# Optimization experiments

Hardware: AMD Instinct MI355X
Metric: run time of the kernel (lower is better)

## Reference

```python
import jax, jax.numpy as jnp
import numpy as np

EMBED_DIM = 768
NUM_HEADS = 12
HEAD_SIZE = EMBED_DIM // NUM_HEADS


def setup_inputs() -> dict:
    key = jax.random.key(0)
    ks = jax.random.split(key, 9)
    B, S, D = 4, 2048, EMBED_DIM
    scale = 1.0 / np.sqrt(D)
    x = jax.random.normal(ks[0], (B, S, D), dtype=jnp.float32)
    # Linear params (torch nn.Linear: y = x @ W.T + b); store W as [in, out] for einsum
    Wq = jax.random.normal(ks[1], (D, D), dtype=jnp.float32) * scale
    bq = jnp.zeros((D,), dtype=jnp.float32)
    Wk = jax.random.normal(ks[2], (D, D), dtype=jnp.float32) * scale
    bk = jnp.zeros((D,), dtype=jnp.float32)
    Wv = jax.random.normal(ks[3], (D, D), dtype=jnp.float32) * scale
    bv = jnp.zeros((D,), dtype=jnp.float32)
    Wo = jax.random.normal(ks[4], (D, D), dtype=jnp.float32) * scale
    bo = jnp.zeros((D,), dtype=jnp.float32)
    return {"x": x, "Wq": Wq, "bq": bq, "Wk": Wk, "bk": bk,
            "Wv": Wv, "bv": bv, "Wo": Wo, "bo": bo}


def reference(x, Wq, bq, Wk, bk, Wv, bv, Wo, bo):
    B, S, D = x.shape
    H, hs = NUM_HEADS, HEAD_SIZE
    scale = hs ** (-0.5)
    # Projections
    Q = (x @ Wq + bq).reshape(B, S, H, hs)
    K = (x @ Wk + bk).reshape(B, S, H, hs)
    V = (x @ Wv + bv).reshape(B, S, H, hs)
    # Batched attention over all heads (equivalent to the per-head loop:
    # torch view splits last dim into H contiguous chunks; concat of per-head
    # outputs along -1 restores the same layout)
    scores = jnp.einsum('bqhd,bkhd->bhqk', Q, K) * scale  # [B,H,S,S]
    attn = jax.nn.softmax(scores, axis=-1)
    out = jnp.einsum('bhqk,bkhd->bqhd', attn, V).reshape(B, S, D)
    # Output projection; dropout is identity in eval mode
    return out @ Wo + bo
```

## Files before the change

### kernel.cpp

```cpp
#include <hip/hip_runtime.h>

typedef unsigned short ushort_t;
typedef __bf16 bf16x8 __attribute__((ext_vector_type(8)));
typedef float floatx4 __attribute__((ext_vector_type(4)));

__device__ inline ushort_t f2bf(float f) {
    __bf16 h = (__bf16)f;
    return __builtin_bit_cast(ushort_t, h);
}

__device__ inline void gload16(const void* g, void* l) {
    __builtin_amdgcn_global_load_lds((const __attribute__((address_space(1))) void*)g,
                                     (__attribute__((address_space(3))) void*)l, 16, 0, 0);
}

__global__ __launch_bounds__(256) void prep_kernel(
    const float* __restrict__ x, ushort_t* __restrict__ xbf,
    const float* __restrict__ W0, const float* __restrict__ W1,
    const float* __restrict__ W2, const float* __restrict__ W3,
    ushort_t* __restrict__ T0, ushort_t* __restrict__ T1,
    ushort_t* __restrict__ T2, ushort_t* __restrict__ T3) {
    int bx = blockIdx.x;
    int tid = threadIdx.x;
    if (bx < 2304) {
        __shared__ float t[32][33];
        int w = bx / 576, rem = bx % 576;
        const float* W; ushort_t* T;
        switch (w) {
            case 0: W = W0; T = T0; break;
            case 1: W = W1; T = T1; break;
            case 2: W = W2; T = T2; break;
            default: W = W3; T = T3; break;
        }
        int n0 = (rem / 24) * 32, k0 = (rem % 24) * 32;
        int tx = tid & 31, ty = tid >> 5;
        for (int i = 0; i < 4; ++i)
            t[ty + i * 8][tx] = W[(k0 + ty + i * 8) * 768 + n0 + tx];
        __syncthreads();
        for (int i = 0; i < 4; ++i)
            T[(n0 + ty + i * 8) * 768 + k0 + tx] = f2bf(t[tx][ty + i * 8]);
    } else {
        int i = ((bx - 2304) * 256 + tid) * 4;
        float4 v = *(const float4*)(x + i);
        ushort4 u;
        u.x = f2bf(v.x); u.y = f2bf(v.y); u.z = f2bf(v.z); u.w = f2bf(v.w);
        *(ushort4*)(xbf + i) = u;
    }
}

__global__ __launch_bounds__(256) void gemm_qkv(
    const ushort_t* __restrict__ A,
    const ushort_t* __restrict__ Tq, const ushort_t* __restrict__ Tk, const ushort_t* __restrict__ Tv,
    const float* __restrict__ bq, const float* __restrict__ bk, const float* __restrict__ bv,
    ushort_t* __restrict__ Qb, ushort_t* __restrict__ Kb, ushort_t* __restrict__ Vtb) {
    __shared__ ushort_t sh[128 * 64 + 64 * 64];
    ushort_t* As = sh;
    ushort_t* Bs = sh + 128 * 64;
    int tid = threadIdx.x;
    int m0 = blockIdx.x * 128;
    int by = blockIdx.y;
    int which = by / 12;
    int n0 = (by % 12) * 64;
    const ushort_t* Bt = which == 0 ? Tq : (which == 1 ? Tk : Tv);
    const float* bias = which == 0 ? bq : (which == 1 ? bk : bv);

    int wave = tid >> 6;
    int lane = tid & 63;
    int ln = tid & 15;
    int quad = (tid >> 4) & 3;
    int wm = wave * 32;
    int lr = lane >> 3;
    int lc = (lane & 7) * 8;

    floatx4 acc[2][4];
    floatx4 z = {0.f, 0.f, 0.f, 0.f};
    for (int i = 0; i < 2; ++i)
        for (int j = 0; j < 4; ++j) acc[i][j] = z;

    for (int kt = 0; kt < 12; ++kt) {
        int k0 = kt * 64;
        __syncthreads();
        for (int i = 0; i < 4; ++i) {
            int c = wave * 4 + i;
            gload16(&A[(m0 + c * 8 + lr) * 768 + k0 + lc], &As[c * 512]);
        }
        for (int i = 0; i < 2; ++i) {
            int c = wave * 2 + i;
            gload16(&Bt[(n0 + c * 8 + lr) * 768 + k0 + lc], &Bs[c * 512]);
        }
        __syncthreads();
        for (int ks = 0; ks < 2; ++ks) {
            bf16x8 a[2], b[4];
            for (int i = 0; i < 2; ++i)
                a[i] = *(const bf16x8*)&As[(wm + i * 16 + ln) * 64 + ks * 32 + quad * 8];
            for (int j = 0; j < 4; ++j)
                b[j] = *(const bf16x8*)&Bs[(j * 16 + ln) * 64 + ks * 32 + quad * 8];
            for (int i = 0; i < 2; ++i)
                for (int j = 0; j < 4; ++j)
                    acc[i][j] = __builtin_amdgcn_mfma_f32_16x16x32_bf16(a[i], b[j], acc[i][j], 0, 0, 0);
        }
    }

    const float QSCALE = 0.125f * 1.44269504088896f;
    if (which != 2) {
        for (int i = 0; i < 2; ++i) {
            for (int j = 0; j < 4; ++j) {
                int gn = n0 + j * 16 + ln;
                float bia = bias[gn];
                int h = gn >> 6, dd = gn & 63;
                for (int r = 0; r < 4; ++r) {
                    int gm = m0 + wm + i * 16 + quad * 4 + r;
                    int bb = gm >> 11, ss = gm & 2047;
                    float v = acc[i][j][r] + bia;
                    if (which == 0) {
                        Qb[((bb * 12 + h) * 2048 + ss) * 64 + dd] = f2bf(v * QSCALE);
                    } else {
                        Kb[((bb * 12 + h) * 2048 + ss) * 64 + dd] = f2bf(v);
                    }
                }
            }
        }
    } else {
        __syncthreads();
        ushort_t* tr = sh;
        for (int j = 0; j < 4; ++j) {
            int nl = j * 16 + ln;
            float bia = bias[n0 + nl];
            for (int i = 0; i < 2; ++i) {
                ushort4 u;
                u.x = f2bf(acc[i][j][0] + bia);
                u.y = f2bf(acc[i][j][1] + bia);
                u.z = f2bf(acc[i][j][2] + bia);
                u.w = f2bf(acc[i][j][3] + bia);
                *(ushort4*)&tr[nl * 136 + wm + i * 16 + quad * 4] = u;
            }
        }
        __syncthreads();
        int bb = m0 >> 11, ss0 = m0 & 2047;
        int head = by % 12;
        for (int p = 0; p < 4; ++p) {
            int n = p * 16 + (tid >> 4);
            int mc = (tid & 15) * 8;
            uint4 v = *(const uint4*)&tr[n * 136 + mc];
            *(uint4*)&Vtb[(size_t)((bb * 12 + head) * 64 + n) * 2048 + ss0 + mc] = v;
        }
    }
}

__global__ __launch_bounds__(256) void attn_kernel(
    const ushort_t* __restrict__ Qb, const ushort_t* __restrict__ Kb,
    const ushort_t* __restrict__ Vtb, ushort_t* __restrict__ Ob) {
    __shared__ ushort_t Ks[2][64 * 72];
    __shared__ ushort_t Vs[2][64 * 72];
    int tid = threadIdx.x;
    int bid = blockIdx.x;
    int swz = (bid & 7) * 96 + (bid >> 3);
    int bh = swz >> 4;
    int qt = swz & 15;
    int wave = tid >> 6;
    int ln = tid & 15;
    int quad = (tid >> 4) & 3;
    int q0 = qt * 128 + wave * 32;

    const ushort_t* Qp = Qb + (size_t)bh * 2048 * 64;
    const ushort_t* Kp = Kb + (size_t)bh * 2048 * 64;
    const ushort_t* Vp = Vtb + (size_t)bh * 64 * 2048;

    bf16x8 bqf[2][2];
    for (int g = 0; g < 2; ++g)
        for (int ks = 0; ks < 2; ++ks)
            bqf[g][ks] = *(const bf16x8*)&Qp[(q0 + g * 16 + ln) * 64 + ks * 32 + quad * 8];

    int srow = tid >> 3;
    int c8 = tid & 7;
    int scol = c8 * 8;
    int u = c8 & 3;
    int vcol = (c8 >> 2) * 32 + (u & 1) * 16 + (u >> 1) * 4;

    uint4 kreg[2], vreg[2];

    for (int p = 0; p < 2; ++p) {
        kreg[p] = *(const uint4*)&Kp[(p * 32 + srow) * 64 + scol];
        vreg[p] = *(const uint4*)&Vp[(p * 32 + srow) * 2048 + scol];
    }
    for (int p = 0; p < 2; ++p) {
        *(uint4*)&Ks[0][(p * 32 + srow) * 72 + scol] = kreg[p];
        ushort_t* vb = &Vs[0][(p * 32 + srow) * 72 + vcol];
        *(uint2*)vb = make_uint2(vreg[p].x, vreg[p].y);
        *(uint2*)(vb + 8) = make_uint2(vreg[p].z, vreg[p].w);
    }
    __syncthreads();

    floatx4 o_acc[2][4];
    float lsum[2] = {0.f, 0.f};
    floatx4 z = {0.f, 0.f, 0.f, 0.f};
    for (int g = 0; g < 2; ++g)
        for (int m4 = 0; m4 < 4; ++m4) o_acc[g][m4] = z;

    for (int kt = 0; kt < 32; ++kt) {
        int cur = kt & 1;
        if (kt < 31) {
            for (int p = 0; p < 2; ++p) {
                kreg[p] = *(const uint4*)&Kp[((kt + 1) * 64 + p * 32 + srow) * 64 + scol];
                vreg[p] = *(const uint4*)&Vp[(p * 32 + srow) * 2048 + (kt + 1) * 64 + scol];
            }
        }

        const ushort_t* KsH = Ks[cur];
        const ushort_t* VsH = Vs[cur];

        bf16x8 ak[4][2];
        for (int m4 = 0; m4 < 4; ++m4)
            for (int ks = 0; ks < 2; ++ks)
                ak[m4][ks] = *(const bf16x8*)&KsH[(m4 * 16 + ln) * 72 + ks * 32 + quad * 8];

        floatx4 st[2][4];
        for (int g = 0; g < 2; ++g)
            for (int m4 = 0; m4 < 4; ++m4) {
                floatx4 s = z;
                s = __builtin_amdgcn_mfma_f32_16x16x32_bf16(ak[m4][0], bqf[g][0], s, 0, 0, 0);
                s = __builtin_amdgcn_mfma_f32_16x16x32_bf16(ak[m4][1], bqf[g][1], s, 0, 0, 0);
                st[g][m4] = s;
            }

        float pv[2][4][4];
        for (int g = 0; g < 2; ++g)
            for (int m4 = 0; m4 < 4; ++m4)
                for (int r = 0; r < 4; ++r) {
                    float e = __builtin_amdgcn_exp2f(st[g][m4][r]);
                    pv[g][m4][r] = e;
                    lsum[g] += e;
                }

        bf16x8 av[4][2];
        for (int m4 = 0; m4 < 4; ++m4)
            for (int c = 0; c < 2; ++c)
                av[m4][c] = *(const bf16x8*)&VsH[(m4 * 16 + ln) * 72 + c * 32 + quad * 8];

        for (int g = 0; g < 2; ++g) {
            bf16x8 bp[2];
            for (int c = 0; c < 2; ++c) {
                bf16x8 b;
                b[0] = (__bf16)pv[g][2 * c][0];
                b[1] = (__bf16)pv[g][2 * c][1];
                b[2] = (__bf16)pv[g][2 * c][2];
                b[3] = (__bf16)pv[g][2 * c][3];
                b[4] = (__bf16)pv[g][2 * c + 1][0];
                b[5] = (__bf16)pv[g][2 * c + 1][1];
                b[6] = (__bf16)pv[g][2 * c + 1][2];
                b[7] = (__bf16)pv[g][2 * c + 1][3];
                bp[c] = b;
            }
            for (int m4 = 0; m4 < 4; ++m4)
                for (int c = 0; c < 2; ++c)
                    o_acc[g][m4] = __builtin_amdgcn_mfma_f32_16x16x32_bf16(av[m4][c], bp[c], o_acc[g][m4], 0, 0, 0);
        }

        if (kt < 31) {
            int nxt = cur ^ 1;
            for (int p = 0; p < 2; ++p) {
                *(uint4*)&Ks[nxt][(p * 32 + srow) * 72 + scol] = kreg[p];
                ushort_t* vb = &Vs[nxt][(p * 32 + srow) * 72 + vcol];
                *(uint2*)vb = make_uint2(vreg[p].x, vreg[p].y);
                *(uint2*)(vb + 8) = make_uint2(vreg[p].z, vreg[p].w);
            }
        }
        __syncthreads();
    }

    for (int g = 0; g < 2; ++g) {
        lsum[g] += __shfl_xor(lsum[g], 16);
        lsum[g] += __shfl_xor(lsum[g], 32);
    }

    int b = bh / 12, h = bh % 12;
    for (int g = 0; g < 2; ++g) {
        float inv = 1.f / lsum[g];
        int token = b * 2048 + q0 + g * 16 + ln;
        for (int m4 = 0; m4 < 4; ++m4)
            for (int r = 0; r < 4; ++r)
                Ob[token * 768 + h * 64 + m4 * 16 + quad * 4 + r] = f2bf(o_acc[g][m4][r] * inv);
    }
}

__global__ __launch_bounds__(256) void gemm_out(
    const ushort_t* __restrict__ A, const ushort_t* __restrict__ Bt,
    const float* __restrict__ bias, float* __restrict__ out) {
    __shared__ ushort_t As[128 * 64];
    __shared__ ushort_t Bs[64 * 64];
    int tid = threadIdx.x;
    int m0 = blockIdx.x * 128;
    int n0 = blockIdx.y * 64;

    int wave = tid >> 6;
    int lane = tid & 63;
    int ln = tid & 15;
    int quad = (tid >> 4) & 3;
    int wm = wave * 32;
    int lr = lane >> 3;
    int lc = (lane & 7) * 8;

    floatx4 acc[2][4];
    floatx4 z = {0.f, 0.f, 0.f, 0.f};
    for (int i = 0; i < 2; ++i)
        for (int j = 0; j < 4; ++j) acc[i][j] = z;

    for (int kt = 0; kt < 12; ++kt) {
        int k0 = kt * 64;
        __syncthreads();
        for (int i = 0; i < 4; ++i) {
            int c = wave * 4 + i;
            gload16(&A[(m0 + c * 8 + lr) * 768 + k0 + lc], &As[c * 512]);
        }
        for (int i = 0; i < 2; ++i) {
            int c = wave * 2 + i;
            gload16(&Bt[(n0 + c * 8 + lr) * 768 + k0 + lc], &Bs[c * 512]);
        }
        __syncthreads();
        for (int ks = 0; ks < 2; ++ks) {
            bf16x8 a[2], b[4];
            for (int i = 0; i < 2; ++i)
                a[i] = *(const bf16x8*)&As[(wm + i * 16 + ln) * 64 + ks * 32 + quad * 8];
            for (int j = 0; j < 4; ++j)
                b[j] = *(const bf16x8*)&Bs[(j * 16 + ln) * 64 + ks * 32 + quad * 8];
            for (int i = 0; i < 2; ++i)
                for (int j = 0; j < 4; ++j)
                    acc[i][j] = __builtin_amdgcn_mfma_f32_16x16x32_bf16(a[i], b[j], acc[i][j], 0, 0, 0);
        }
    }

    for (int i = 0; i < 2; ++i) {
        for (int j = 0; j < 4; ++j) {
            int gn = n0 + j * 16 + ln;
            float bia = bias[gn];
            for (int r = 0; r < 4; ++r) {
                int gm = m0 + wm + i * 16 + quad * 4 + r;
                out[gm * 768 + gn] = acc[i][j][r] + bia;
            }
        }
    }
}

extern "C" void kernel_launch(void* const* d_in, const int* in_sizes, int n_in,
                              void* d_out, int out_size, void* d_ws, size_t ws_size,
                              hipStream_t stream) {
    const float* x  = (const float*)d_in[0];
    const float* Wq = (const float*)d_in[1];
    const float* bq = (const float*)d_in[2];
    const float* Wk = (const float*)d_in[3];
    const float* bk = (const float*)d_in[4];
    const float* Wv = (const float*)d_in[5];
    const float* bv = (const float*)d_in[6];
    const float* Wo = (const float*)d_in[7];
    const float* bo = (const float*)d_in[8];

    const int NTOK = 4 * 2048;
    const int NELT = NTOK * 768;
    const int WELT = 768 * 768;

    ushort_t* xbf = (ushort_t*)d_ws;
    ushort_t* Tq  = xbf + NELT;
    ushort_t* Tk  = Tq + WELT;
    ushort_t* Tv  = Tk + WELT;
    ushort_t* To  = Tv + WELT;
    ushort_t* Qb  = To + WELT;
    ushort_t* Kb  = Qb + NELT;
    ushort_t* Vtb = Kb + NELT;
    ushort_t* Ob  = Vtb + NELT;

    prep_kernel<<<8448, 256, 0, stream>>>(x, xbf, Wq, Wk, Wv, Wo, Tq, Tk, Tv, To);
    gemm_qkv<<<dim3(64, 36), 256, 0, stream>>>(xbf, Tq, Tk, Tv, bq, bk, bv, Qb, Kb, Vtb);
    attn_kernel<<<768, 256, 0, stream>>>(Qb, Kb, Vtb, Ob);
    gemm_out<<<dim3(64, 12), 256, 0, stream>>>(Ob, To, bo, (float*)d_out);
}
```

Baseline: 222.2 us.

## Split attention key tile across wave pairs and reduce partial outputs in LDS

Reorganizes the attention kernel's four waves into 2 query groups × 2 key halves. Each wave now handles 64 queries against 32 of the 64 keys per tile, which halves the per-wave LDS fragment reads of K and V while keeping the MFMA count the same. After the loop, the second key-half wave writes its partial output and row sums into reused shared memory, and the first wave combines them and normalizes. The cost is doubled Q and accumulator registers per wave and an extra LDS reduction with a barrier. The float scratch buffer reaches past the Ks array into Vs, so it relies on the two arrays being laid out contiguously.

```diff
diff --git a/kernel.cpp b/kernel.cpp
--- a/kernel.cpp
+++ b/kernel.cpp
@@ -158,16 +158,18 @@
     int bh = swz >> 4;
     int qt = swz & 15;
     int wave = tid >> 6;
+    int qh = wave >> 1;
+    int kh = wave & 1;
     int ln = tid & 15;
     int quad = (tid >> 4) & 3;
-    int q0 = qt * 128 + wave * 32;
+    int q0 = qt * 128 + qh * 64;
 
     const ushort_t* Qp = Qb + (size_t)bh * 2048 * 64;
     const ushort_t* Kp = Kb + (size_t)bh * 2048 * 64;
     const ushort_t* Vp = Vtb + (size_t)bh * 64 * 2048;
 
-    bf16x8 bqf[2][2];
-    for (int g = 0; g < 2; ++g)
+    bf16x8 bqf[4][2];
+    for (int g = 0; g < 4; ++g)
         for (int ks = 0; ks < 2; ++ks)
             bqf[g][ks] = *(const bf16x8*)&Qp[(q0 + g * 16 + ln) * 64 + ks * 32 + quad * 8];
 
@@ -191,10 +193,10 @@
     }
     __syncthreads();
 
-    floatx4 o_acc[2][4];
-    float lsum[2] = {0.f, 0.f};
+    floatx4 o_acc[4][4];
+    float lsum[4] = {0.f, 0.f, 0.f, 0.f};
     floatx4 z = {0.f, 0.f, 0.f, 0.f};
-    for (int g = 0; g < 2; ++g)
+    for (int g = 0; g < 4; ++g)
         for (int m4 = 0; m4 < 4; ++m4) o_acc[g][m4] = z;
 
     for (int kt = 0; kt < 32; ++kt) {
@@ -209,51 +211,45 @@
         const ushort_t* KsH = Ks[cur];
         const ushort_t* VsH = Vs[cur];
 
-        bf16x8 ak[4][2];
-        for (int m4 = 0; m4 < 4; ++m4)
+        bf16x8 ak[2][2];
+        for (int m = 0; m < 2; ++m)
             for (int ks = 0; ks < 2; ++ks)
-                ak[m4][ks] = *(const bf16x8*)&KsH[(m4 * 16 + ln) * 72 + ks * 32 + quad * 8];
-
-        floatx4 st[2][4];
-        for (int g = 0; g < 2; ++g)
-            for (int m4 = 0; m4 < 4; ++m4) {
+                ak[m][ks] = *(const bf16x8*)&KsH[((kh * 2 + m) * 16 + ln) * 72 + ks * 32 + quad * 8];
+
+        floatx4 st[4][2];
+        for (int g = 0; g < 4; ++g)
+            for (int m = 0; m < 2; ++m) {
                 floatx4 s = z;
-                s = __builtin_amdgcn_mfma_f32_16x16x32_bf16(ak[m4][0], bqf[g][0], s, 0, 0, 0);
-                s = __builtin_amdgcn_mfma_f32_16x16x32_bf16(ak[m4][1], bqf[g][1], s, 0, 0, 0);
-                st[g][m4] = s;
-            }
-
-        float pv[2][4][4];
-        for (int g = 0; g < 2; ++g)
-            for (int m4 = 0; m4 < 4; ++m4)
+                s = __builtin_amdgcn_mfma_f32_16x16x32_bf16(ak[m][0], bqf[g][0], s, 0, 0, 0);
+                s = __builtin_amdgcn_mfma_f32_16x16x32_bf16(ak[m][1], bqf[g][1], s, 0, 0, 0);
+                st[g][m] = s;
+            }
+
+        float pv[4][2][4];
+        for (int g = 0; g < 4; ++g)
+            for (int m = 0; m < 2; ++m)
                 for (int r = 0; r < 4; ++r) {
-                    float e = __builtin_amdgcn_exp2f(st[g][m4][r]);
-                    pv[g][m4][r] = e;
+                    float e = __builtin_amdgcn_exp2f(st[g][m][r]);
+                    pv[g][m][r] = e;
                     lsum[g] += e;
                 }
 
-        bf16x8 av[4][2];
+        bf16x8 av[4];
         for (int m4 = 0; m4 < 4; ++m4)
-            for (int c = 0; c < 2; ++c)
-                av[m4][c] = *(const bf16x8*)&VsH[(m4 * 16 + ln) * 72 + c * 32 + quad * 8];
-
-        for (int g = 0; g < 2; ++g) {
-            bf16x8 bp[2];
-            for (int c = 0; c < 2; ++c) {
-                bf16x8 b;
-                b[0] = (__bf16)pv[g][2 * c][0];
-                b[1] = (__bf16)pv[g][2 * c][1];
-                b[2] = (__bf16)pv[g][2 * c][2];
-                b[3] = (__bf16)pv[g][2 * c][3];
-                b[4] = (__bf16)pv[g][2 * c + 1][0];
-                b[5] = (__bf16)pv[g][2 * c + 1][1];
-                b[6] = (__bf16)pv[g][2 * c + 1][2];
-                b[7] = (__bf16)pv[g][2 * c + 1][3];
-                bp[c] = b;
-            }
+            av[m4] = *(const bf16x8*)&VsH[(m4 * 16 + ln) * 72 + kh * 32 + quad * 8];
+
+        for (int g = 0; g < 4; ++g) {
+            bf16x8 b;
+            b[0] = (__bf16)pv[g][0][0];
+            b[1] = (__bf16)pv[g][0][1];
+            b[2] = (__bf16)pv[g][0][2];
+            b[3] = (__bf16)pv[g][0][3];
+            b[4] = (__bf16)pv[g][1][0];
+            b[5] = (__bf16)pv[g][1][1];
+            b[6] = (__bf16)pv[g][1][2];
+            b[7] = (__bf16)pv[g][1][3];
             for (int m4 = 0; m4 < 4; ++m4)
-                for (int c = 0; c < 2; ++c)
-                    o_acc[g][m4] = __builtin_amdgcn_mfma_f32_16x16x32_bf16(av[m4][c], bp[c], o_acc[g][m4], 0, 0, 0);
+                o_acc[g][m4] = __builtin_amdgcn_mfma_f32_16x16x32_bf16(av[m4], b, o_acc[g][m4], 0, 0, 0);
         }
 
         if (kt < 31) {
@@ -268,18 +264,36 @@
         __syncthreads();
     }
 
-    for (int g = 0; g < 2; ++g) {
+    for (int g = 0; g < 4; ++g) {
         lsum[g] += __shfl_xor(lsum[g], 16);
         lsum[g] += __shfl_xor(lsum[g], 32);
     }
 
+    float* mbuf = (float*)&Ks[0][0];
+    float* lbuf = mbuf + 2 * 64 * 68;
+    if (kh == 1) {
+        float* base = mbuf + qh * 64 * 68;
+        for (int g = 0; g < 4; ++g) {
+            for (int m4 = 0; m4 < 4; ++m4)
+                *(floatx4*)&base[(g * 16 + ln) * 68 + m4 * 16 + quad * 4] = o_acc[g][m4];
+            if (quad == 0) lbuf[qh * 64 + g * 16 + ln] = lsum[g];
+        }
+    }
+    __syncthreads();
+
     int b = bh / 12, h = bh % 12;
-    for (int g = 0; g < 2; ++g) {
-        float inv = 1.f / lsum[g];
-        int token = b * 2048 + q0 + g * 16 + ln;
-        for (int m4 = 0; m4 < 4; ++m4)
-            for (int r = 0; r < 4; ++r)
-                Ob[token * 768 + h * 64 + m4 * 16 + quad * 4 + r] = f2bf(o_acc[g][m4][r] * inv);
+    if (kh == 0) {
+        float* base = mbuf + qh * 64 * 68;
+        for (int g = 0; g < 4; ++g) {
+            float inv = 1.f / (lsum[g] + lbuf[qh * 64 + g * 16 + ln]);
+            int token = b * 2048 + q0 + g * 16 + ln;
+            for (int m4 = 0; m4 < 4; ++m4) {
+                floatx4 o2 = *(const floatx4*)&base[(g * 16 + ln) * 68 + m4 * 16 + quad * 4];
+                for (int r = 0; r < 4; ++r)
+                    Ob[token * 768 + h * 64 + m4 * 16 + quad * 4 + r] =
+                        f2bf((o_acc[g][m4][r] + o2[r]) * inv);
+            }
+        }
     }
 }
 
```

Result: slower. 281.2 us (+26.5%).
